# Kernel tuning notes

Hardware: AMD Instinct MI355X
Metric: run time of the kernel (lower is better)

Reference implementation:

```python
import jax, jax.numpy as jnp
import numpy as np

EPS = 1e-8  # torch F.cosine_similarity default eps


def setup_inputs() -> dict:
    key = jax.random.key(0)
    k1, k2 = jax.random.split(key)
    xs_pad = jax.random.normal(k1, (8, 4096, 512), dtype=jnp.float32)
    spk_emb = jax.random.normal(k2, (8, 256, 512), dtype=jnp.float32)
    return {"xs_pad": xs_pad, "spk_emb": spk_emb}


def reference(xs_pad, spk_emb):
    # Faithful to F.cosine_similarity(x.unsqueeze(2), y.unsqueeze(1), dim=-1):
    #   dot(x, y) / (max(||x||, eps) * max(||y||, eps))
    # Implemented as L2-normalize then a batched GEMM -> (B, T, S), avoiding
    # the (B, T, S, D) broadcast intermediate.
    x_norm = jnp.maximum(jnp.linalg.norm(xs_pad, axis=-1, keepdims=True), EPS)
    y_norm = jnp.maximum(jnp.linalg.norm(spk_emb, axis=-1, keepdims=True), EPS)
    xn = xs_pad / x_norm          # (B, T, D)
    yn = spk_emb / y_norm         # (B, S, D)
    scores = jnp.einsum('btd,bsd->bts', xn, yn)  # (B, T, S)
    return scores
```

## Files before the change

### kernel.cpp

```cpp
#include <hip/hip_runtime.h>
#include <hip/hip_bf16.h>

#define BB 8
#define TT 4096
#define SS 256
#define DD 512

typedef __attribute__((ext_vector_type(8))) short short8;
typedef __attribute__((ext_vector_type(4))) float floatx4;

__device__ inline short f2bf(float f) {
  unsigned u = __builtin_bit_cast(unsigned, f);
  u += 0x7fffu + ((u >> 16) & 1u);
  return (short)(u >> 16);
}

__device__ inline short8 cvt8(float4 f0, float4 f1) {
  short8 o;
  o[0] = f2bf(f0.x);
  o[1] = f2bf(f0.y);
  o[2] = f2bf(f0.z);
  o[3] = f2bf(f0.w);
  o[4] = f2bf(f1.x);
  o[5] = f2bf(f1.y);
  o[6] = f2bf(f1.z);
  o[7] = f2bf(f1.w);
  return o;
}

__device__ inline float sq8(float4 f0, float4 f1) {
  return f0.x * f0.x + f0.y * f0.y + f0.z * f0.z + f0.w * f0.w +
         f1.x * f1.x + f1.y * f1.y + f1.z * f1.z + f1.w * f1.w;
}

__global__ __launch_bounds__(256) void cos_fused_kernel(
    const float* __restrict__ xs, const float* __restrict__ spk,
    float* __restrict__ out) {
  __shared__ float sA[128 * 64];
  __shared__ float sB[128 * 64];
  __shared__ float scX[128];
  __shared__ float scY[128];

  const int tid = threadIdx.x;
  const int wave = tid >> 6;
  const int lane = tid & 63;
  const int tn = blockIdx.x;
  const int tm = blockIdx.y;
  const int b = blockIdx.z;

  const float* Abase = xs + ((size_t)b * TT + tm * 128) * DD;
  const float* Bbase = spk + ((size_t)b * SS + tn * 128) * DD;

  floatx4 acc[4][4];
#pragma unroll
  for (int i = 0; i < 4; i++)
#pragma unroll
    for (int j = 0; j < 4; j++) acc[i][j] = (floatx4){0.f, 0.f, 0.f, 0.f};

  float sx[4] = {0.f, 0.f, 0.f, 0.f};
  float sy[4] = {0.f, 0.f, 0.f, 0.f};

  const int wm = wave >> 1;
  const int wn = wave & 1;
  const int quad = lane >> 4;
  const int l15 = lane & 15;

  int aoff[8];
#pragma unroll
  for (int j = 0; j < 8; j++) {
    int s = j * 256 + tid;
    int row = s >> 4;
    int blk = (s & 15) ^ (row & 15);
    aoff[j] = row * DD + blk * 4;
  }

  for (int kt = 0; kt < DD / 64; ++kt) {
#pragma unroll
    for (int j = 0; j < 8; j++) {
      const float* ga = Abase + aoff[j] + kt * 64;
      const float* gb = Bbase + aoff[j] + kt * 64;
      __builtin_amdgcn_global_load_lds(
          (const __attribute__((address_space(1))) unsigned int*)ga,
          (__attribute__((address_space(3))) unsigned int*)(sA +
              (j * 256 + wave * 64) * 4),
          16, 0, 0);
      __builtin_amdgcn_global_load_lds(
          (const __attribute__((address_space(1))) unsigned int*)gb,
          (__attribute__((address_space(3))) unsigned int*)(sB +
              (j * 256 + wave * 64) * 4),
          16, 0, 0);
    }
    __syncthreads();

#pragma unroll
    for (int ks = 0; ks < 2; ks++) {
      short8 af[4], bf[4];
      const int b0 = ks * 8 + quad * 2;
#pragma unroll
      for (int im = 0; im < 4; im++) {
        int row = wm * 64 + im * 16 + l15;
        int s0 = b0 ^ (row & 15);
        int s1 = (b0 + 1) ^ (row & 15);
        float4 f0 = *(const float4*)(sA + row * 64 + s0 * 4);
        float4 f1 = *(const float4*)(sA + row * 64 + s1 * 4);
        sx[im] += sq8(f0, f1);
        af[im] = cvt8(f0, f1);
      }
#pragma unroll
      for (int in = 0; in < 4; in++) {
        int row = wn * 64 + in * 16 + l15;
        int s0 = b0 ^ (row & 15);
        int s1 = (b0 + 1) ^ (row & 15);
        float4 f0 = *(const float4*)(sB + row * 64 + s0 * 4);
        float4 f1 = *(const float4*)(sB + row * 64 + s1 * 4);
        sy[in] += sq8(f0, f1);
        bf[in] = cvt8(f0, f1);
      }
#pragma unroll
      for (int im = 0; im < 4; im++)
#pragma unroll
        for (int in = 0; in < 4; in++)
          acc[im][in] = __builtin_amdgcn_mfma_f32_16x16x32_bf16(
              af[im], bf[in], acc[im][in], 0, 0, 0);
    }
    __syncthreads();
  }

#pragma unroll
  for (int i = 0; i < 4; i++) {
    sx[i] += __shfl_xor(sx[i], 16, 64);
    sx[i] += __shfl_xor(sx[i], 32, 64);
    sy[i] += __shfl_xor(sy[i], 16, 64);
    sy[i] += __shfl_xor(sy[i], 32, 64);
  }
  if (quad == 0) {
#pragma unroll
    for (int i = 0; i < 4; i++) {
      scX[wm * 64 + i * 16 + l15] = 1.0f / fmaxf(sqrtf(sx[i]), 1e-8f);
      scY[wn * 64 + i * 16 + l15] = 1.0f / fmaxf(sqrtf(sy[i]), 1e-8f);
    }
  }
  __syncthreads();

  float* Obase = out + ((size_t)b * TT + tm * 128) * SS + tn * 128;
#pragma unroll
  for (int im = 0; im < 4; im++) {
#pragma unroll
    for (int in = 0; in < 4; in++) {
      int col = wn * 64 + in * 16 + l15;
      float yv = scY[col];
#pragma unroll
      for (int r = 0; r < 4; r++) {
        int row = wm * 64 + im * 16 + quad * 4 + r;
        Obase[row * SS + col] = acc[im][in][r] * scX[row] * yv;
      }
    }
  }
}

extern "C" void kernel_launch(void* const* d_in, const int* in_sizes, int n_in,
                              void* d_out, int out_size, void* d_ws,
                              size_t ws_size, hipStream_t stream) {
  const float* xs = (const float*)d_in[0];
  const float* spk = (const float*)d_in[1];
  float* out = (float*)d_out;

  hipLaunchKernelGGL(cos_fused_kernel, dim3(SS / 128, TT / 128, BB), dim3(256),
                     0, stream, xs, spk, out);
}
```

Before: 123.8 us.

## Compute row norms via Gram MFMA diagonals and use packed bf16 conversion

Drops the per-element FP32 sum-of-squares accumulation for the x and y row norms. Each wave instead issues extra MFMAs multiplying a fragment by itself and reads the squared norms off the diagonal of that Gram block. Waves on the diagonal (wm==wn) cover the A rows and the others cover the B rows. The float-to-bf16 conversion also switches to the paired intrinsic. This adds four MFMAs per k-step per wave to save VALU work, but the norms now come from bf16-rounded values, which slightly reduces their accuracy.

```diff
diff --git a/kernel.cpp b/kernel.cpp
--- a/kernel.cpp
+++ b/kernel.cpp
@@ -8,29 +8,22 @@
 
 typedef __attribute__((ext_vector_type(8))) short short8;
 typedef __attribute__((ext_vector_type(4))) float floatx4;
+typedef __attribute__((ext_vector_type(4))) int intx4;
 
-__device__ inline short f2bf(float f) {
-  unsigned u = __builtin_bit_cast(unsigned, f);
-  u += 0x7fffu + ((u >> 16) & 1u);
-  return (short)(u >> 16);
+__device__ inline int pk2(float a, float b) {
+  __hip_bfloat162 h = __float22bfloat162_rn(make_float2(a, b));
+  int r;
+  __builtin_memcpy(&r, &h, 4);
+  return r;
 }
 
 __device__ inline short8 cvt8(float4 f0, float4 f1) {
-  short8 o;
-  o[0] = f2bf(f0.x);
-  o[1] = f2bf(f0.y);
-  o[2] = f2bf(f0.z);
-  o[3] = f2bf(f0.w);
-  o[4] = f2bf(f1.x);
-  o[5] = f2bf(f1.y);
-  o[6] = f2bf(f1.z);
-  o[7] = f2bf(f1.w);
-  return o;
-}
-
-__device__ inline float sq8(float4 f0, float4 f1) {
-  return f0.x * f0.x + f0.y * f0.y + f0.z * f0.z + f0.w * f0.w +
-         f1.x * f1.x + f1.y * f1.y + f1.z * f1.z + f1.w * f1.w;
+  intx4 p;
+  p[0] = pk2(f0.x, f0.y);
+  p[1] = pk2(f0.z, f0.w);
+  p[2] = pk2(f1.x, f1.y);
+  p[3] = pk2(f1.z, f1.w);
+  return __builtin_bit_cast(short8, p);
 }
 
 __global__ __launch_bounds__(256) void cos_fused_kernel(
@@ -56,14 +49,15 @@
   for (int i = 0; i < 4; i++)
 #pragma unroll
     for (int j = 0; j < 4; j++) acc[i][j] = (floatx4){0.f, 0.f, 0.f, 0.f};
-
-  float sx[4] = {0.f, 0.f, 0.f, 0.f};
-  float sy[4] = {0.f, 0.f, 0.f, 0.f};
+  floatx4 accG[4];
+#pragma unroll
+  for (int i = 0; i < 4; i++) accG[i] = (floatx4){0.f, 0.f, 0.f, 0.f};
 
   const int wm = wave >> 1;
   const int wn = wave & 1;
   const int quad = lane >> 4;
   const int l15 = lane & 15;
+  const bool gramA = (wm == wn);
 
   int aoff[8];
 #pragma unroll
@@ -103,7 +97,6 @@
         int s1 = (b0 + 1) ^ (row & 15);
         float4 f0 = *(const float4*)(sA + row * 64 + s0 * 4);
         float4 f1 = *(const float4*)(sA + row * 64 + s1 * 4);
-        sx[im] += sq8(f0, f1);
         af[im] = cvt8(f0, f1);
       }
 #pragma unroll
@@ -113,7 +106,6 @@
         int s1 = (b0 + 1) ^ (row & 15);
         float4 f0 = *(const float4*)(sB + row * 64 + s0 * 4);
         float4 f1 = *(const float4*)(sB + row * 64 + s1 * 4);
-        sy[in] += sq8(f0, f1);
         bf[in] = cvt8(f0, f1);
       }
 #pragma unroll
@@ -122,22 +114,29 @@
         for (int in = 0; in < 4; in++)
           acc[im][in] = __builtin_amdgcn_mfma_f32_16x16x32_bf16(
               af[im], bf[in], acc[im][in], 0, 0, 0);
+      if (gramA) {
+#pragma unroll
+        for (int im = 0; im < 4; im++)
+          accG[im] = __builtin_amdgcn_mfma_f32_16x16x32_bf16(
+              af[im], af[im], accG[im], 0, 0, 0);
+      } else {
+#pragma unroll
+        for (int in = 0; in < 4; in++)
+          accG[in] = __builtin_amdgcn_mfma_f32_16x16x32_bf16(
+              bf[in], bf[in], accG[in], 0, 0, 0);
+      }
     }
     __syncthreads();
   }
 
-#pragma unroll
-  for (int i = 0; i < 4; i++) {
-    sx[i] += __shfl_xor(sx[i], 16, 64);
-    sx[i] += __shfl_xor(sx[i], 32, 64);
-    sy[i] += __shfl_xor(sy[i], 16, 64);
-    sy[i] += __shfl_xor(sy[i], 32, 64);
-  }
-  if (quad == 0) {
+  if (quad == (l15 >> 2)) {
 #pragma unroll
     for (int i = 0; i < 4; i++) {
-      scX[wm * 64 + i * 16 + l15] = 1.0f / fmaxf(sqrtf(sx[i]), 1e-8f);
-      scY[wn * 64 + i * 16 + l15] = 1.0f / fmaxf(sqrtf(sy[i]), 1e-8f);
+      float inv = 1.0f / fmaxf(sqrtf(accG[i][l15 & 3]), 1e-8f);
+      if (gramA)
+        scX[wm * 64 + i * 16 + l15] = inv;
+      else
+        scY[wn * 64 + i * 16 + l15] = inv;
     }
   }
   __syncthreads();
```

After: 122.2 us. About the same (-1.3%).
